# Kernel tuning notes

Measured on AMD Instinct MI355X. Metric: run time of the kernel, lower is better.

The kernel has to match this reference:

```python
import jax, jax.numpy as jnp
import numpy as np

B, N, M = 32, 8400, 32
NUM_CLASSES = 80
TOP_K = 10
CLS_W, OBJ_W, REG_W = 1.0, 1.0, 5.0
EPS = 1e-7
IMG = 640.0


def setup_inputs() -> dict:
    key = jax.random.key(0)
    k1, k2, k3, k4, k5, k6, k7 = jax.random.split(key, 7)
    # decoded predictions in pixel scale: [cx, cy, w, h, obj_logit, cls_logits...]
    cxy = jax.random.uniform(k1, (B, N, 2), jnp.float32, 0.0, IMG)
    wh = jax.random.uniform(k2, (B, N, 2), jnp.float32, 10.0, 110.0)
    obj = jax.random.normal(k3, (B, N, 1), jnp.float32)
    cls = jax.random.normal(k4, (B, N, NUM_CLASSES), jnp.float32)
    predictions = jnp.concatenate([cxy, wh, obj, cls], axis=-1)  # (B, N, 85)
    # targets: [cls, cx, cy, w, h]
    gcls = jnp.floor(jax.random.uniform(k5, (B, M, 1), jnp.float32, 0.0, float(NUM_CLASSES)))
    gxy = jax.random.uniform(k6, (B, M, 2), jnp.float32, 50.0, IMG - 50.0)
    gwh = jax.random.uniform(k7, (B, M, 2), jnp.float32, 20.0, 120.0)
    targets = jnp.concatenate([gcls, gxy, gwh], axis=-1)  # (B, M, 5)
    return {"predictions": predictions, "targets": targets}


def cxcywh_to_xyxy(b):
    cx, cy, w, h = b[..., 0], b[..., 1], b[..., 2], b[..., 3]
    return jnp.stack([cx - w / 2, cy - h / 2, cx + w / 2, cy + h / 2], axis=-1)


def bce_with_logits(x, t):
    # numerically stable elementwise BCE with logits
    return jnp.maximum(x, 0.0) - x * t + jnp.log1p(jnp.exp(-jnp.abs(x)))


def pairwise_iou(g, p):
    # g: (M,4) xyxy, p: (N,4) xyxy -> (M,N)
    ix1 = jnp.maximum(g[:, None, 0], p[None, :, 0])
    iy1 = jnp.maximum(g[:, None, 1], p[None, :, 1])
    ix2 = jnp.minimum(g[:, None, 2], p[None, :, 2])
    iy2 = jnp.minimum(g[:, None, 3], p[None, :, 3])
    inter = jnp.clip(ix2 - ix1, 0.0) * jnp.clip(iy2 - iy1, 0.0)
    ga = jnp.clip(g[:, 2] - g[:, 0], 0.0) * jnp.clip(g[:, 3] - g[:, 1], 0.0)
    pa = jnp.clip(p[:, 2] - p[:, 0], 0.0) * jnp.clip(p[:, 3] - p[:, 1], 0.0)
    union = ga[:, None] + pa[None, :] - inter + EPS
    return inter / union


def giou(pred, tgt):
    # elementwise GIoU, pred/tgt (N,4) xyxy -> (N,)
    ix1 = jnp.maximum(pred[:, 0], tgt[:, 0]); iy1 = jnp.maximum(pred[:, 1], tgt[:, 1])
    ix2 = jnp.minimum(pred[:, 2], tgt[:, 2]); iy2 = jnp.minimum(pred[:, 3], tgt[:, 3])
    inter = jnp.clip(ix2 - ix1, 0.0) * jnp.clip(iy2 - iy1, 0.0)
    pa = jnp.clip(pred[:, 2] - pred[:, 0], 0.0) * jnp.clip(pred[:, 3] - pred[:, 1], 0.0)
    ta = jnp.clip(tgt[:, 2] - tgt[:, 0], 0.0) * jnp.clip(tgt[:, 3] - tgt[:, 1], 0.0)
    union = pa + ta - inter + EPS
    iou = inter / union
    ex1 = jnp.minimum(pred[:, 0], tgt[:, 0]); ey1 = jnp.minimum(pred[:, 1], tgt[:, 1])
    ex2 = jnp.maximum(pred[:, 2], tgt[:, 2]); ey2 = jnp.maximum(pred[:, 3], tgt[:, 3])
    enclose = (ex2 - ex1) * (ey2 - ey1) + EPS
    return iou - (enclose - union) / enclose


def _image_loss(pred, tgt):
    # pred: (N, 5+C), tgt: (M, 5)
    pbox = pred[:, :4]
    obj_logit = pred[:, 4]
    cls_logit = pred[:, 5:]
    pxyxy = cxcywh_to_xyxy(pbox)
    gcls = tgt[:, 0].astype(jnp.int32)                  # (M,)
    gxyxy = cxcywh_to_xyxy(tgt[:, 1:5])                 # (M,4)

    iou = pairwise_iou(gxyxy, pxyxy)                    # (M,N)

    # center prior: anchor (prediction) centers inside GT boxes
    cx, cy = pbox[:, 0], pbox[:, 1]
    in_box = ((cx[None, :] > gxyxy[:, 0:1]) & (cx[None, :] < gxyxy[:, 2:3]) &
              (cy[None, :] > gxyxy[:, 1:2]) & (cy[None, :] < gxyxy[:, 3:4]))  # (M,N)

    # classification cost: BCE(sqrt(cls_p*obj_p), onehot), decomposed to avoid (M,N,C)
    score = jnp.sqrt(jax.nn.sigmoid(cls_logit) * jax.nn.sigmoid(obj_logit)[:, None])  # (N,C)
    lp = jnp.log(score + EPS)
    lq = jnp.log(1.0 - score + EPS)
    base = -lq.sum(axis=-1)                             # (N,) = sum_c BCE(p, 0)
    cost_cls = base[None, :] - lp[:, gcls].T + lq[:, gcls].T  # (M,N)

    reg_cost = -jnp.log(iou + 1e-8)
    cost = cost_cls + 3.0 * reg_cost + 1e5 * (~in_box).astype(pred.dtype)
    cost = jax.lax.stop_gradient(cost)

    # dynamic-k: k_m = clip(sum of top-k IoUs, min 1)
    iou_sg = jax.lax.stop_gradient(iou) * in_box.astype(pred.dtype)
    topk_ious, _ = jax.lax.top_k(iou_sg, TOP_K)         # (M, TOP_K)
    dyn_k = jnp.clip(topk_ious.sum(-1).astype(jnp.int32), 1, None)  # (M,)

    # per-GT: keep the dyn_k lowest-cost candidates (rank via double argsort)
    ranks = jnp.argsort(jnp.argsort(cost, axis=1), axis=1)
    assigned = (ranks < dyn_k[:, None]) & in_box        # (M,N)

    # conflict resolution: anchor keeps only its lowest-cost GT
    big = jnp.asarray(1e30, pred.dtype)
    cost_masked = jnp.where(assigned, cost, big)
    matched_gt = jnp.argmin(cost_masked, axis=0)        # (N,)
    fg = assigned.any(axis=0)                            # (N,)
    fgf = fg.astype(pred.dtype)

    # objectness loss over all anchors
    obj_l = bce_with_logits(obj_logit, fgf).sum()
    # classification loss on foreground anchors
    onehot = jax.nn.one_hot(gcls[matched_gt], NUM_CLASSES, dtype=pred.dtype)
    cls_l = (bce_with_logits(cls_logit, onehot) * fgf[:, None]).sum()
    mbox = gxyxy[matched_gt]                            # (N,4)
    reg_l = ((1.0 - giou(pxyxy, mbox)) * fgf).sum()
    return cls_l, obj_l, reg_l, fgf.sum()


def reference(predictions, targets):
    cls_l, obj_l, reg_l, nfg = jax.vmap(_image_loss)(predictions, targets)
    num_fg = jnp.maximum(nfg.sum(), 1.0)
    total = (CLS_W * cls_l.sum() + OBJ_W * obj_l.sum() + REG_W * reg_l.sum()) / num_fg
    return total
```

## Files before the change

### kernel.cpp

```cpp
#include <hip/hip_runtime.h>
#include <math.h>

#define BB 32
#define NN 8400
#define MM 32
#define NC 80
#define PD 85
#define TOPK 10
#define CAPG 768
#define KPL 12
#define NBLK 1050
#define FLT_BIG 3.4e38f

__device__ __forceinline__ float frcp_(float x)  { return __builtin_amdgcn_rcpf(x); }
__device__ __forceinline__ float fsqrt_(float x) { return __builtin_amdgcn_sqrtf(x); }
__device__ __forceinline__ float fsig_(float x)  { return frcp_(1.0f + __expf(-x)); }

__device__ __forceinline__ float bcef_(float x, float t) {
    return fmaxf(x, 0.0f) - x * t + __logf(1.0f + __expf(-fabsf(x)));
}

__device__ __forceinline__ float iou_(float4 pb, float gx1, float gy1,
                                      float gx2, float gy2, float ga) {
    float ix1 = fmaxf(gx1, pb.x), iy1 = fmaxf(gy1, pb.y);
    float ix2 = fminf(gx2, pb.z), iy2 = fminf(gy2, pb.w);
    float inter = fmaxf(ix2 - ix1, 0.0f) * fmaxf(iy2 - iy1, 0.0f);
    float pa = fmaxf(pb.z - pb.x, 0.0f) * fmaxf(pb.w - pb.y, 0.0f);
    float uni = ga + pa - inter + 1e-7f;
    return inter * frcp_(uni);
}
__device__ __forceinline__ float cost_(float cl, float so_n, float base_n, float iou) {
    float s = fsqrt_(fsig_(cl) * so_n);
    float lp = __logf(s + 1e-7f);
    float lq = __logf(1.0f - s + 1e-7f);
    return base_n - lp + lq - 3.0f * __logf(iou + 1e-8f);
}

__global__ void __launch_bounds__(256) kA(const float* __restrict__ pred,
                                          const float* __restrict__ tgt,
                                          float4* __restrict__ pxyxy,
                                          float* __restrict__ base,
                                          float* __restrict__ so,
                                          float* __restrict__ objlogit,
                                          unsigned int* __restrict__ inmask,
                                          unsigned int* __restrict__ mask) {
    const int tid = threadIdx.x;
    const int lane = tid & 63, wid = tid >> 6;
    const int rs = lane >> 5, g = lane & 31;
    const int b = blockIdx.y;
    const int tile = blockIdx.x;

    const float* t = tgt + ((size_t)b * MM + g) * 5;
    const float gx1 = t[1] - t[3] * 0.5f, gy1 = t[2] - t[4] * 0.5f;
    const float gx2 = t[1] + t[3] * 0.5f, gy2 = t[2] + t[4] * 0.5f;

    for (int itr = 0; itr < 2; ++itr) {
        const int pl = wid * 2 + itr;
        const int r0 = tile * 16 + pl * 2;
        const size_t off = ((size_t)b * NN + r0) * PD;

        float x0 = pred[off + lane];
        float x1 = pred[off + 64 + lane];

        float cx0 = __shfl(x0, 0), cy0 = __shfl(x0, 1), w0 = __shfl(x0, 2), h0 = __shfl(x0, 3), ol0 = __shfl(x0, 4);
        float cx1 = __shfl(x1, 21), cy1 = __shfl(x1, 22), w1 = __shfl(x1, 23), h1 = __shfl(x1, 24), ol1 = __shfl(x1, 25);
        float so0 = fsig_(ol0), so1 = fsig_(ol1);

        const float cxs = rs ? cx1 : cx0, cys = rs ? cy1 : cy0;
        const bool inb = (cxs > gx1) && (cxs < gx2) && (cys > gy1) && (cys < gy2);
        const unsigned long long bal = __ballot(inb);
        const bool r0a = (bal & 0xFFFFFFFFull) != 0ull;
        const bool r1a = (bal >> 32) != 0ull;

        const size_t gi = (size_t)b * NN + r0;
        if (lane == 0) {
            pxyxy[gi] = make_float4(cx0 - w0 * 0.5f, cy0 - h0 * 0.5f,
                                    cx0 + w0 * 0.5f, cy0 + h0 * 0.5f);
            objlogit[gi] = ol0; so[gi] = so0;
        } else if (lane == 1) {
            pxyxy[gi + 1] = make_float4(cx1 - w1 * 0.5f, cy1 - h1 * 0.5f,
                                        cx1 + w1 * 0.5f, cy1 + h1 * 0.5f);
            objlogit[gi + 1] = ol1; so[gi + 1] = so1;
        } else if (lane == 2) mask[gi] = 0u;
        else if (lane == 3) mask[gi + 1] = 0u;
        else if (lane == 4) inmask[gi] = (unsigned int)(bal & 0xFFFFFFFFull);
        else if (lane == 5) inmask[gi + 1] = (unsigned int)(bal >> 32);

        if (r0a) {
            float a0 = 0.0f;
            if (lane >= 5)  a0 += __logf(1.0f - fsqrt_(fsig_(x0) * so0) + 1e-7f);
            if (lane < 21)  a0 += __logf(1.0f - fsqrt_(fsig_(x1) * so0) + 1e-7f);
            #pragma unroll
            for (int o = 32; o; o >>= 1) a0 += __shfl_xor(a0, o);
            if (lane == 0) base[gi] = -a0;
        }
        if (r1a) {
            float x2 = (lane < 42) ? pred[off + 128 + lane] : 0.0f;
            float a1 = 0.0f;
            if (lane >= 26) a1 += __logf(1.0f - fsqrt_(fsig_(x1) * so1) + 1e-7f);
            if (lane < 42)  a1 += __logf(1.0f - fsqrt_(fsig_(x2) * so1) + 1e-7f);
            #pragma unroll
            for (int o = 32; o; o >>= 1) a1 += __shfl_xor(a1, o);
            if (lane == 0) base[gi + 1] = -a1;
        }
    }
}

__global__ void __launch_bounds__(256) kC(const float* __restrict__ pred,
                                          const float* __restrict__ tgt,
                                          const float4* __restrict__ pxyxy,
                                          const float* __restrict__ base,
                                          const float* __restrict__ so,
                                          const unsigned int* __restrict__ inmask,
                                          unsigned int* __restrict__ mask) {
    const int x_ = blockIdx.x & 7, k_ = blockIdx.x >> 3;
    const int g = k_ & 31, b = ((k_ >> 5) << 3) | x_;
    const int tid = threadIdx.x;
    const int wid = tid >> 6, lane = tid & 63;

    const float* t = tgt + ((size_t)b * MM + g) * 5;
    const int gcls = (int)t[0];
    const float gx1 = t[1] - t[3] * 0.5f, gy1 = t[2] - t[4] * 0.5f;
    const float gx2 = t[1] + t[3] * 0.5f, gy2 = t[2] + t[4] * 0.5f;
    const float ga = fmaxf(gx2 - gx1, 0.0f) * fmaxf(gy2 - gy1, 0.0f);
    const size_t nb = (size_t)b * NN;
    const unsigned int gbit = 1u << g;

    __shared__ float s_iou[CAPG];
    __shared__ float s_cost[CAPG];
    __shared__ int   s_n[CAPG];
    __shared__ int   s_cnt;
    if (tid == 0) s_cnt = 0;
    __syncthreads();

    #define KC_BODY(nn_)                                                       \
        do { int n = (nn_);                                                    \
            float4 pb = pxyxy[nb + n];                                         \
            float iou = iou_(pb, gx1, gy1, gx2, gy2, ga);                      \
            float cl = pred[(nb + (size_t)n) * PD + 5 + gcls];                 \
            float co = cost_(cl, so[nb + n], base[nb + n], iou);               \
            int idx = atomicAdd(&s_cnt, 1);                                    \
            if (idx < CAPG) { s_iou[idx] = iou; s_cost[idx] = co; s_n[idx] = n; } \
        } while (0)

    for (int n4 = tid; n4 < NN; n4 += 1024) {
        unsigned int m0 = inmask[nb + n4];
        unsigned int m1 = (n4 + 256 < NN) ? inmask[nb + n4 + 256] : 0u;
        unsigned int m2 = (n4 + 512 < NN) ? inmask[nb + n4 + 512] : 0u;
        unsigned int m3 = (n4 + 768 < NN) ? inmask[nb + n4 + 768] : 0u;
        if (m0 & gbit) KC_BODY(n4);
        if (m1 & gbit) KC_BODY(n4 + 256);
        if (m2 & gbit) KC_BODY(n4 + 512);
        if (m3 & gbit) KC_BODY(n4 + 768);
    }
    #undef KC_BODY
    __syncthreads();

    if (wid != 0) return;
    const int cnt = min(s_cnt, CAPG);

    float riou[KPL], rcost[KPL]; int rn[KPL];
    #pragma unroll
    for (int k = 0; k < KPL; ++k) {
        int i = lane + 64 * k;
        bool v = i < cnt;
        riou[k]  = v ? s_iou[i]  : -1.0f;
        rcost[k] = v ? s_cost[i] : FLT_BIG;
        rn[k]    = v ? s_n[i]    : 0x7fffffff;
    }

    float ssum = 0.0f;
    {
        const int lim = (cnt < TOPK) ? cnt : TOPK;
        for (int p = 0; p < lim; ++p) {
            float bv = -1.0f; int bidx = 0x7fffffff;
            #pragma unroll
            for (int k = 0; k < KPL; ++k)
                if (riou[k] > bv) { bv = riou[k]; bidx = lane + 64 * k; }
            #pragma unroll
            for (int o = 32; o; o >>= 1) {
                float ov = __shfl_xor(bv, o); int oi = __shfl_xor(bidx, o);
                if (ov > bv || (ov == bv && oi < bidx)) { bv = ov; bidx = oi; }
            }
            ssum += bv;
            if ((bidx & 63) == lane) {
                int kk = bidx >> 6;
                #pragma unroll
                for (int k = 0; k < KPL; ++k) if (k == kk) riou[k] = -1.0f;
            }
        }
    }
    int dynk = (int)ssum;
    if (dynk < 1) dynk = 1;
    if (dynk > TOPK) dynk = TOPK;

    {
        const int lim = (cnt < dynk) ? cnt : dynk;
        for (int p = 0; p < lim; ++p) {
            float bv = FLT_BIG; int bn_ = 0x7fffffff; int bidx = -1;
            #pragma unroll
            for (int k = 0; k < KPL; ++k)
                if (rcost[k] < bv || (rcost[k] == bv && rn[k] < bn_)) {
                    bv = rcost[k]; bn_ = rn[k]; bidx = lane + 64 * k;
                }
            #pragma unroll
            for (int o = 32; o; o >>= 1) {
                float ov = __shfl_xor(bv, o);
                int on = __shfl_xor(bn_, o);
                int oi = __shfl_xor(bidx, o);
                if (ov < bv || (ov == bv && on < bn_)) { bv = ov; bn_ = on; bidx = oi; }
            }
            if ((bidx & 63) == lane) {
                int kk = bidx >> 6;
                #pragma unroll
                for (int k = 0; k < KPL; ++k)
                    if (k == kk) { rcost[k] = FLT_BIG; rn[k] = 0x7fffffff; }
            }
            if (lane == 0) atomicOr(&mask[nb + bn_], gbit);
        }
    }
}

__global__ void __launch_bounds__(256) kD(const float* __restrict__ pred,
                   const float* __restrict__ tgt,
                   const float4* __restrict__ pxyxy,
                   const float* __restrict__ base,
                   const float* __restrict__ so,
                   const float* __restrict__ objlogit,
                   const unsigned int* __restrict__ mask,
                   float* __restrict__ partials) {
    const int tid = threadIdx.x;
    const int i0 = blockIdx.x * 256;
    const int i = i0 + tid;
    const int lane = tid & 63, wid = tid >> 6;
    const int b = i / NN;

    float obj_l, cls_l = 0.0f, reg_l = 0.0f, nfg = 0.0f;
    const unsigned int mk = mask[i];
    obj_l = bcef_(objlogit[i], mk ? 1.0f : 0.0f);

    __shared__ int s_list[256];
    __shared__ int s_gcls[256];
    __shared__ int s_wbase[4];
    __shared__ int s_cnt;

    unsigned long long bal = __ballot(mk != 0);
    int wpos = __popcll(bal & ((1ull << lane) - 1ull));
    if (lane == 0) s_wbase[wid] = __popcll(bal);
    __syncthreads();
    if (tid == 0) {
        int acc = 0;
        for (int w = 0; w < 4; ++w) { int t_ = s_wbase[w]; s_wbase[w] = acc; acc += t_; }
        s_cnt = acc;
    }
    __syncthreads();

    if (mk) {
        int e = s_wbase[wid] + wpos;
        s_list[e] = tid;
        nfg = 1.0f;
        float4 pb = pxyxy[i];
        float base_n = base[i], so_n = so[i];
        float best = 3.0e30f; int bg = 0;
        unsigned int m = mk;
        while (m) {
            int g = __ffs(m) - 1;
            m &= m - 1;
            const float* tg = tgt + ((size_t)b * MM + g) * 5;
            float ggx1 = tg[1] - tg[3] * 0.5f, ggy1 = tg[2] - tg[4] * 0.5f;
            float ggx2 = tg[1] + tg[3] * 0.5f, ggy2 = tg[2] + tg[4] * 0.5f;
            float gga = fmaxf(ggx2 - ggx1, 0.0f) * fmaxf(ggy2 - ggy1, 0.0f);
            float iou = iou_(pb, ggx1, ggy1, ggx2, ggy2, gga);
            float cl = pred[(size_t)i * PD + 5 + (int)tg[0]];
            float cvv = cost_(cl, so_n, base_n, iou);
            if (cvv < best) { best = cvv; bg = g; }
        }
        const float* tm = tgt + ((size_t)b * MM + bg) * 5;
        s_gcls[e] = (int)tm[0];
        float px1 = pb.x, py1 = pb.y, px2 = pb.z, py2 = pb.w;
        float tx1 = tm[1] - tm[3] * 0.5f, ty1 = tm[2] - tm[4] * 0.5f;
        float tx2 = tm[1] + tm[3] * 0.5f, ty2 = tm[2] + tm[4] * 0.5f;
        float ix1 = fmaxf(px1, tx1), iy1 = fmaxf(py1, ty1);
        float ix2 = fminf(px2, tx2), iy2 = fminf(py2, ty2);
        float inter = fmaxf(ix2 - ix1, 0.0f) * fmaxf(iy2 - iy1, 0.0f);
        float pa = fmaxf(px2 - px1, 0.0f) * fmaxf(py2 - py1, 0.0f);
        float ta = fmaxf(tx2 - tx1, 0.0f) * fmaxf(ty2 - ty1, 0.0f);
        float uni = pa + ta - inter + 1e-7f;
        float iou = inter / uni;
        float ex1 = fminf(px1, tx1), ey1 = fminf(py1, ty1);
        float ex2 = fmaxf(px2, tx2), ey2 = fmaxf(py2, ty2);
        float enclose = (ex2 - ex1) * (ey2 - ey1) + 1e-7f;
        float giou = iou - (enclose - uni) / enclose;
        reg_l = 1.0f - giou;
    }
    __syncthreads();

    const int cnt = s_cnt;
    const int nitems = cnt * NC;
    for (int item = tid; item < nitems; item += 256) {
        int e = item / NC;
        int c = item - e * NC;
        int gi = i0 + s_list[e];
        float x = pred[(size_t)gi * PD + 5 + c];
        cls_l += bcef_(x, (c == s_gcls[e]) ? 1.0f : 0.0f);
    }

    float sums[4] = {cls_l, obj_l, reg_l, nfg};
    #pragma unroll
    for (int j = 0; j < 4; ++j)
        #pragma unroll
        for (int o = 32; o; o >>= 1) sums[j] += __shfl_xor(sums[j], o);
    __shared__ float sred[16];
    if (lane == 0) {
        sred[wid * 4 + 0] = sums[0]; sred[wid * 4 + 1] = sums[1];
        sred[wid * 4 + 2] = sums[2]; sred[wid * 4 + 3] = sums[3];
    }
    __syncthreads();
    if (tid == 0) {
        float* pr = partials + (size_t)blockIdx.x * 4;
        #pragma unroll
        for (int j = 0; j < 4; ++j)
            pr[j] = sred[j] + sred[4 + j] + sred[8 + j] + sred[12 + j];
    }
}

__global__ void kE(const float* __restrict__ partials, int nblk, float* __restrict__ out) {
    __shared__ float red[256];
    float s[4] = {0, 0, 0, 0};
    for (int i = threadIdx.x; i < nblk; i += 256) {
        s[0] += partials[(size_t)i * 4 + 0];
        s[1] += partials[(size_t)i * 4 + 1];
        s[2] += partials[(size_t)i * 4 + 2];
        s[3] += partials[(size_t)i * 4 + 3];
    }
    float tot[4];
    for (int j = 0; j < 4; ++j) {
        red[threadIdx.x] = s[j];
        __syncthreads();
        for (int off = 128; off > 0; off >>= 1) {
            if (threadIdx.x < off) red[threadIdx.x] += red[threadIdx.x + off];
            __syncthreads();
        }
        tot[j] = red[0];
        __syncthreads();
    }
    if (threadIdx.x == 0) {
        float nfg = fmaxf(tot[3], 1.0f);
        out[0] = (tot[0] + tot[1] + 5.0f * tot[2]) / nfg;
    }
}

extern "C" void kernel_launch(void* const* d_in, const int* in_sizes, int n_in,
                              void* d_out, int out_size, void* d_ws, size_t ws_size,
                              hipStream_t stream) {
    const float* pred = (const float*)d_in[0];
    const float* tgt  = (const float*)d_in[1];
    float* out = (float*)d_out;

    char* ws = (char*)d_ws;
    size_t off = 0;
    float4* pxyxy = (float4*)(ws + off);            off += (size_t)BB * NN * sizeof(float4);
    float* base = (float*)(ws + off);               off += (size_t)BB * NN * sizeof(float);
    float* so = (float*)(ws + off);                 off += (size_t)BB * NN * sizeof(float);
    float* objlogit = (float*)(ws + off);           off += (size_t)BB * NN * sizeof(float);
    unsigned int* inmask = (unsigned int*)(ws + off); off += (size_t)BB * NN * sizeof(unsigned int);
    unsigned int* mask = (unsigned int*)(ws + off); off += (size_t)BB * NN * sizeof(unsigned int);
    float* partials = (float*)(ws + off);           off += (size_t)NBLK * 4 * sizeof(float);

    dim3 gA(NN / 16, BB);
    kA<<<gA, 256, 0, stream>>>(pred, tgt, pxyxy, base, so, objlogit, inmask, mask);

    kC<<<MM * BB, 256, 0, stream>>>(pred, tgt, pxyxy, base, so, inmask, mask);

    kD<<<NBLK, 256, 0, stream>>>(pred, tgt, pxyxy, base, so, objlogit, mask, partials);

    kE<<<1, 256, 0, stream>>>(partials, NBLK, out);
}
```

Before: 85.38 us.

## Restructure kA to thread-per-anchor in-box test with compacted active-anchor base pass

kA now assigns one thread per anchor, testing its center against all 32 GT boxes cached in shared memory to build the in-box mask. Anchors inside at least one box are compacted into a shared list via ballot and prefix sum, and one wavefront per active anchor then computes the base class-cost sum. This replaces the old scheme where each wavefront handled two anchors at a time with mostly idle lanes. The goal is better lane utilisation and fewer per-lane branches in the header stage, at the cost of extra block barriers and a second strided read of active anchor rows.

```diff
diff --git a/kernel.cpp b/kernel.cpp
--- a/kernel.cpp
+++ b/kernel.cpp
@@ -46,63 +46,69 @@
                                           unsigned int* __restrict__ mask) {
     const int tid = threadIdx.x;
     const int lane = tid & 63, wid = tid >> 6;
-    const int rs = lane >> 5, g = lane & 31;
     const int b = blockIdx.y;
-    const int tile = blockIdx.x;
-
-    const float* t = tgt + ((size_t)b * MM + g) * 5;
-    const float gx1 = t[1] - t[3] * 0.5f, gy1 = t[2] - t[4] * 0.5f;
-    const float gx2 = t[1] + t[3] * 0.5f, gy2 = t[2] + t[4] * 0.5f;
-
-    for (int itr = 0; itr < 2; ++itr) {
-        const int pl = wid * 2 + itr;
-        const int r0 = tile * 16 + pl * 2;
-        const size_t off = ((size_t)b * NN + r0) * PD;
-
+    const int r = blockIdx.x * 256 + tid;
+
+    __shared__ float4 sg[MM];
+    __shared__ int s_act[256];
+    __shared__ int s_wb[4];
+    __shared__ int s_na;
+
+    if (tid < MM) {
+        const float* t = tgt + ((size_t)b * MM + tid) * 5;
+        sg[tid] = make_float4(t[1] - t[3] * 0.5f, t[2] - t[4] * 0.5f,
+                              t[1] + t[3] * 0.5f, t[2] + t[4] * 0.5f);
+    }
+    __syncthreads();
+
+    const bool valid = r < NN;
+    unsigned int im = 0u;
+    if (valid) {
+        const size_t gi = (size_t)b * NN + r;
+        const float* p = pred + gi * PD;
+        float4 h4 = *reinterpret_cast<const float4*>(p);
+        float ol = p[4];
+        float cx = h4.x, cy = h4.y, w = h4.z, h = h4.w;
+        #pragma unroll
+        for (int g = 0; g < MM; ++g) {
+            float4 gb = sg[g];
+            bool inb = (cx > gb.x) && (cx < gb.z) && (cy > gb.y) && (cy < gb.w);
+            im |= inb ? (1u << g) : 0u;
+        }
+        pxyxy[gi] = make_float4(cx - w * 0.5f, cy - h * 0.5f,
+                                cx + w * 0.5f, cy + h * 0.5f);
+        objlogit[gi] = ol;
+        so[gi] = fsig_(ol);
+        inmask[gi] = im;
+        mask[gi] = 0u;
+    }
+
+    unsigned long long bal = __ballot(valid && im != 0u);
+    int wpos = __popcll(bal & ((1ull << lane) - 1ull));
+    if (lane == 0) s_wb[wid] = __popcll(bal);
+    __syncthreads();
+    if (tid == 0) {
+        int acc = 0;
+        for (int w2 = 0; w2 < 4; ++w2) { int t2 = s_wb[w2]; s_wb[w2] = acc; acc += t2; }
+        s_na = acc;
+    }
+    __syncthreads();
+    if (valid && im != 0u) s_act[s_wb[wid] + wpos] = r;
+    __syncthreads();
+
+    const int na = s_na;
+    for (int idx = wid; idx < na; idx += 4) {
+        const int ar = s_act[idx];
+        const size_t off = ((size_t)b * NN + ar) * PD;
         float x0 = pred[off + lane];
-        float x1 = pred[off + 64 + lane];
-
-        float cx0 = __shfl(x0, 0), cy0 = __shfl(x0, 1), w0 = __shfl(x0, 2), h0 = __shfl(x0, 3), ol0 = __shfl(x0, 4);
-        float cx1 = __shfl(x1, 21), cy1 = __shfl(x1, 22), w1 = __shfl(x1, 23), h1 = __shfl(x1, 24), ol1 = __shfl(x1, 25);
-        float so0 = fsig_(ol0), so1 = fsig_(ol1);
-
-        const float cxs = rs ? cx1 : cx0, cys = rs ? cy1 : cy0;
-        const bool inb = (cxs > gx1) && (cxs < gx2) && (cys > gy1) && (cys < gy2);
-        const unsigned long long bal = __ballot(inb);
-        const bool r0a = (bal & 0xFFFFFFFFull) != 0ull;
-        const bool r1a = (bal >> 32) != 0ull;
-
-        const size_t gi = (size_t)b * NN + r0;
-        if (lane == 0) {
-            pxyxy[gi] = make_float4(cx0 - w0 * 0.5f, cy0 - h0 * 0.5f,
-                                    cx0 + w0 * 0.5f, cy0 + h0 * 0.5f);
-            objlogit[gi] = ol0; so[gi] = so0;
-        } else if (lane == 1) {
-            pxyxy[gi + 1] = make_float4(cx1 - w1 * 0.5f, cy1 - h1 * 0.5f,
-                                        cx1 + w1 * 0.5f, cy1 + h1 * 0.5f);
-            objlogit[gi + 1] = ol1; so[gi + 1] = so1;
-        } else if (lane == 2) mask[gi] = 0u;
-        else if (lane == 3) mask[gi + 1] = 0u;
-        else if (lane == 4) inmask[gi] = (unsigned int)(bal & 0xFFFFFFFFull);
-        else if (lane == 5) inmask[gi + 1] = (unsigned int)(bal >> 32);
-
-        if (r0a) {
-            float a0 = 0.0f;
-            if (lane >= 5)  a0 += __logf(1.0f - fsqrt_(fsig_(x0) * so0) + 1e-7f);
-            if (lane < 21)  a0 += __logf(1.0f - fsqrt_(fsig_(x1) * so0) + 1e-7f);
-            #pragma unroll
-            for (int o = 32; o; o >>= 1) a0 += __shfl_xor(a0, o);
-            if (lane == 0) base[gi] = -a0;
-        }
-        if (r1a) {
-            float x2 = (lane < 42) ? pred[off + 128 + lane] : 0.0f;
-            float a1 = 0.0f;
-            if (lane >= 26) a1 += __logf(1.0f - fsqrt_(fsig_(x1) * so1) + 1e-7f);
-            if (lane < 42)  a1 += __logf(1.0f - fsqrt_(fsig_(x2) * so1) + 1e-7f);
-            #pragma unroll
-            for (int o = 32; o; o >>= 1) a1 += __shfl_xor(a1, o);
-            if (lane == 0) base[gi + 1] = -a1;
-        }
+        float x1 = (lane < 21) ? pred[off + 64 + lane] : 0.0f;
+        float so_r = fsig_(__shfl(x0, 4));
+        float a = 0.0f;
+        if (lane >= 5) a += __logf(1.0f - fsqrt_(fsig_(x0) * so_r) + 1e-7f);
+        if (lane < 21) a += __logf(1.0f - fsqrt_(fsig_(x1) * so_r) + 1e-7f);
+        #pragma unroll
+        for (int o = 32; o; o >>= 1) a += __shfl_xor(a, o);
+        if (lane == 0) base[(size_t)b * NN + ar] = -a;
     }
 }
 
@@ -367,7 +373,7 @@
     unsigned int* mask = (unsigned int*)(ws + off); off += (size_t)BB * NN * sizeof(unsigned int);
     float* partials = (float*)(ws + off);           off += (size_t)NBLK * 4 * sizeof(float);
 
-    dim3 gA(NN / 16, BB);
+    dim3 gA((NN + 255) / 256, BB);
     kA<<<gA, 256, 0, stream>>>(pred, tgt, pxyxy, base, so, objlogit, inmask, mask);
 
     kC<<<MM * BB, 256, 0, stream>>>(pred, tgt, pxyxy, base, so, inmask, mask);
```

Measured after the change: 82.89 us. 2.9% less time.
